# Optimization experiments

Measured on AMD Instinct MI355X. Metric: run time of the kernel, lower is better.

## Reference

```python
import jax, jax.numpy as jnp
import numpy as np

B, T, D, H = 4, 2048, 1024, 16
HD = D // H  # 64
NEG = -np.finfo(np.float32).max


def setup_inputs() -> dict:
    key = jax.random.key(0)
    ks = jax.random.split(key, 9)
    s = 1.0 / np.sqrt(D)
    return {
        "x": jax.random.normal(ks[0], (B, T, D), jnp.float32),
        "wq": jax.random.normal(ks[1], (D, D), jnp.float32) * s,
        "bq": jax.random.normal(ks[2], (D,), jnp.float32) * 0.02,
        "wk": jax.random.normal(ks[3], (D, D), jnp.float32) * s,
        "bk": jax.random.normal(ks[4], (D,), jnp.float32) * 0.02,
        "wv": jax.random.normal(ks[5], (D, D), jnp.float32) * s,
        "bv": jax.random.normal(ks[6], (D,), jnp.float32) * 0.02,
        "wo": jax.random.normal(ks[7], (D, D), jnp.float32) * s,
        "bo": jax.random.normal(ks[8], (D,), jnp.float32) * 0.02,
    }


def reference(x, wq, bq, wk, bk, wv, bv, wo, bo):
    b, t, d = x.shape
    # separate Q, K, V projections, reshape to (B, H, T, HD)
    def proj(w, bias):
        y = x @ w + bias
        return y.reshape(b, t, H, HD).transpose(0, 2, 1, 3)
    q = proj(wq, bq)
    k = proj(wk, bk)
    v = proj(wv, bv)
    scale = 1.0 / np.sqrt(HD).astype(np.float32)
    scores = jnp.einsum("bhqd,bhkd->bhqk", q, k) * scale  # (B,H,T,T)
    # causal mask: -max_float on strictly upper triangle (matches source)
    mask = jnp.triu(jnp.full((t, t), NEG, jnp.float32), k=1)
    attn = jax.nn.softmax(scores + mask, axis=-1)
    out = jnp.einsum("bhqk,bhkd->bhqd", attn, v)
    out = out.transpose(0, 2, 1, 3).reshape(b, t, d)
    return out @ wo + bo
```

## Files before the change

kernel.cpp:

```cpp
#include <hip/hip_runtime.h>

typedef __bf16 bf16x8 __attribute__((ext_vector_type(8)));
typedef float f32x4 __attribute__((ext_vector_type(4)));

#define B_ 4
#define T_ 2048
#define D_ 1024
#define H_ 16
#define HD_ 64
#define M_ 8192
#define QSCALE 0.1803368801111204f

__device__ __forceinline__ ushort f2b(float f) {
  union { float f; unsigned u; } v; v.f = f;
  unsigned u = v.u;
  return (ushort)((u + 0x7FFFu + ((u >> 16) & 1u)) >> 16);
}

__device__ __forceinline__ unsigned pkbf(float a, float b) {
  union { float f; unsigned u; } va, vb; va.f = a; vb.f = b;
  return __builtin_amdgcn_perm(vb.u + 0x8000u, va.u + 0x8000u, 0x07060302u);
}

__device__ __forceinline__ void gll16(const void* g, void* l) {
  __builtin_amdgcn_global_load_lds(
      (const __attribute__((address_space(1))) unsigned*)g,
      (__attribute__((address_space(3))) unsigned*)l, 16, 0, 0);
}

__global__ __launch_bounds__(256) void cast_x_kernel(const float* __restrict__ x,
                                                     ushort* __restrict__ xb) {
  int idx = blockIdx.x * 256 + threadIdx.x;
  float4 v = ((const float4*)x)[idx];
  ushort4 o;
  o.x = f2b(v.x); o.y = f2b(v.y); o.z = f2b(v.z); o.w = f2b(v.w);
  ((ushort4*)xb)[idx] = o;
}

__global__ __launch_bounds__(256) void transpose_w_kernel(
    const float* __restrict__ wq, const float* __restrict__ wk,
    const float* __restrict__ wv, const float* __restrict__ wo,
    ushort* __restrict__ wt_qkv, ushort* __restrict__ wt_o) {
  __shared__ float tile[32][33];
  int z = blockIdx.z;
  const float* src = (z == 0) ? wq : (z == 1) ? wk : (z == 2) ? wv : wo;
  ushort* dst = (z < 3) ? (wt_qkv + (size_t)z * D_ * D_) : wt_o;
  int n0 = blockIdx.x * 32, k0 = blockIdx.y * 32;
  int tx = threadIdx.x & 31, ty = threadIdx.x >> 5;
  for (int i = 0; i < 4; i++) {
    int r = ty + i * 8;
    tile[r][tx] = src[(size_t)(k0 + r) * D_ + n0 + tx];
  }
  __syncthreads();
  for (int i = 0; i < 4; i++) {
    int r = ty + i * 8;
    dst[(size_t)(n0 + r) * D_ + k0 + tx] = f2b(tile[tx][r]);
  }
}

__global__ __launch_bounds__(256) void gemm_kernel(
    const ushort* __restrict__ A, const ushort* __restrict__ Bt, int mode,
    const float* __restrict__ bias_q, const float* __restrict__ bias_k,
    const float* __restrict__ bias_v,
    ushort* __restrict__ qb, ushort* __restrict__ kb, ushort* __restrict__ vtb,
    float* __restrict__ outf) {
  __shared__ ushort As[2][128][64];
  __shared__ ushort Bs[2][128][64];
  int tid = threadIdx.x;
  int wave = tid >> 6, lane = tid & 63, lrow = lane >> 4, lcol = lane & 15;

  int gx = gridDim.x;
  int nwg = gx * gridDim.y;
  int orig = blockIdx.x + gx * blockIdx.y;
  int work = (orig & 7) * (nwg >> 3) + (orig >> 3);
  int m0 = (work / gx) * 128, n0 = (work % gx) * 128;
  int wm = (wave & 1) * 64, wn = (wave >> 1) * 64;

  int rb = tid >> 3;
  int dc = tid & 7;
  int scv = dc ^ (rb & 7);
  const ushort* aBase = A + (size_t)(m0 + rb) * D_ + scv * 8;
  const ushort* bBase = Bt + (size_t)(n0 + rb) * D_ + scv * 8;

  f32x4 zero = {0.f, 0.f, 0.f, 0.f};
  f32x4 acc[4][4];
  for (int i = 0; i < 4; i++)
    for (int j = 0; j < 4; j++) acc[i][j] = zero;

  int swz = lcol & 7;

  auto stage = [&](int buf, int k) {
#pragma unroll
    for (int g = 0; g < 4; g++) {
      gll16(aBase + (size_t)(32 * g) * D_ + k, &As[buf][0][0] + tid * 8 + g * 2048);
      gll16(bBase + (size_t)(32 * g) * D_ + k, &Bs[buf][0][0] + tid * 8 + g * 2048);
    }
  };

  stage(0, 0);

  for (int k0 = 0; k0 < D_; k0 += 64) {
    int cur = (k0 >> 6) & 1, nxt = cur ^ 1;
    __syncthreads();
    if (k0 + 64 < D_) stage(nxt, k0 + 64);

    for (int ks = 0; ks < 2; ks++) {
      bf16x8 af[4], bf[4];
      int ch = ((ks * 4 + lrow) ^ swz) * 8;
      for (int mt = 0; mt < 4; mt++)
        af[mt] = *(const bf16x8*)&As[cur][wm + mt * 16 + lcol][ch];
      for (int nt = 0; nt < 4; nt++)
        bf[nt] = *(const bf16x8*)&Bs[cur][wn + nt * 16 + lcol][ch];
      for (int mt = 0; mt < 4; mt++)
        for (int nt = 0; nt < 4; nt++)
          acc[mt][nt] = __builtin_amdgcn_mfma_f32_16x16x32_bf16(
              af[mt], bf[nt], acc[mt][nt], 0, 0, 0);
    }
  }

  if (mode == 0) {
    int proj = n0 >> 10;
    const float* bias = (proj == 0) ? bias_q : (proj == 1) ? bias_k : bias_v;
    if (proj < 2) {
      ushort* dst = (proj == 0) ? qb : kb;
      bool isq = (proj == 0);
      int c0 = lcol & 1, c1 = lcol & 2;
      for (int mt = 0; mt < 4; mt++) {
        int gm0 = m0 + wm + mt * 16 + lrow * 4;
        int t = gm0 + (lcol & 3);
        int b = t >> 11, tp = t & 2047;
        for (int nt = 0; nt < 4; nt++) {
          int gn = n0 + wn + nt * 16 + lcol;
          int inner = gn & 1023;
          float bv = bias[inner];
          float v0 = acc[mt][nt][0] + bv, v1 = acc[mt][nt][1] + bv;
          float v2 = acc[mt][nt][2] + bv, v3 = acc[mt][nt][3] + bv;
          if (isq) { v0 *= QSCALE; v1 *= QSCALE; v2 *= QSCALE; v3 *= QSCALE; }
          unsigned p0 = ((unsigned)f2b(v1) << 16) | f2b(v0);
          unsigned p1 = ((unsigned)f2b(v3) << 16) | f2b(v2);
          unsigned x0 = __shfl_xor(p0, 1), x1 = __shfl_xor(p1, 1);
          unsigned a0 = c0 ? __builtin_amdgcn_perm(p0, x0, 0x07060302u)
                           : __builtin_amdgcn_perm(x0, p0, 0x05040100u);
          unsigned a1 = c0 ? __builtin_amdgcn_perm(p1, x1, 0x07060302u)
                           : __builtin_amdgcn_perm(x1, p1, 0x05040100u);
          unsigned y0 = __shfl_xor(a0, 2), y1 = __shfl_xor(a1, 2);
          uint2 q2;
          q2.x = c1 ? y1 : a0;
          q2.y = c1 ? a1 : y0;
          int innerb = (n0 + wn + nt * 16 + (lcol & ~3)) & 1023;
          int h = innerb >> 6, hd0 = innerb & 63;
          *(uint2*)&dst[((size_t)(b * H_ + h) * T_ + tp) * HD_ + hd0] = q2;
        }
      }
    } else {
      for (int mt = 0; mt < 4; mt++) {
        int gm0 = m0 + wm + mt * 16 + lrow * 4;
        int b = gm0 >> 11, tp = gm0 & 2047;
        for (int nt = 0; nt < 4; nt++) {
          int gn = n0 + wn + nt * 16 + lcol;
          int inner = gn & 1023;
          int h = inner >> 6, hd = inner & 63;
          float bv = bias[inner];
          ushort4 pk;
          pk.x = f2b(acc[mt][nt][0] + bv);
          pk.y = f2b(acc[mt][nt][1] + bv);
          pk.z = f2b(acc[mt][nt][2] + bv);
          pk.w = f2b(acc[mt][nt][3] + bv);
          *(ushort4*)&vtb[((size_t)(b * H_ + h) * HD_ + hd) * T_ + tp] = pk;
        }
      }
    }
  } else {
    for (int mt = 0; mt < 4; mt++) {
      int gm0 = m0 + wm + mt * 16 + lrow * 4;
      for (int nt = 0; nt < 4; nt++) {
        int gn = n0 + wn + nt * 16 + lcol;
        float bv = bias_q[gn];
        for (int r = 0; r < 4; r++)
          outf[(size_t)(gm0 + r) * D_ + gn] = acc[mt][nt][r] + bv;
      }
    }
  }
}

#define QCOMP(qblk_, q0w_, qfv, accOv, accSv)                                   \
  do {                                                                          \
    f32x4 st[2][4];                                                             \
    for (int qh = 0; qh < 2; qh++)                                              \
      for (int mt = 0; mt < 4; mt++) st[qh][mt] = zero;                         \
    __builtin_amdgcn_s_setprio(1);                                              \
    _Pragma("unroll")                                                           \
    for (int ks = 0; ks < 2; ks++)                                              \
      _Pragma("unroll")                                                         \
      for (int mt = 0; mt < 4; mt++) {                                          \
        bf16x8 kf = *(const bf16x8*)&Ks2[cur][mt * 16 + lcol]                   \
                                        [((ks * 4 + lrow) ^ rsw) * 8];          \
        st[0][mt] = __builtin_amdgcn_mfma_f32_16x16x32_bf16(kf, qfv[0][ks],     \
                                                            st[0][mt], 0, 0, 0);\
        st[1][mt] = __builtin_amdgcn_mfma_f32_16x16x32_bf16(kf, qfv[1][ks],     \
                                                            st[1][mt], 0, 0, 0);\
      }                                                                         \
    __builtin_amdgcn_s_setprio(0);                                              \
    if (j >= 2 * (qblk_)) {                                                     \
      _Pragma("unroll")                                                         \
      for (int qh = 0; qh < 2; qh++) {                                          \
        int q_g = (q0w_) + qh * 16 + lcol;                                      \
        _Pragma("unroll")                                                       \
        for (int mt = 0; mt < 4; mt++)                                          \
          for (int r = 0; r < 4; r++) {                                         \
            int kv_g = j * 64 + mt * 16 + lrow * 4 + r;                         \
            if (kv_g > q_g) st[qh][mt][r] = -1e30f;                             \
          }                                                                     \
      }                                                                         \
    }                                                                           \
    _Pragma("unroll")                                                           \
    for (int qh = 0; qh < 2; qh++)                                              \
      for (int mt = 0; mt < 4; mt++)                                            \
        for (int r = 0; r < 4; r++)                                             \
          st[qh][mt][r] = __builtin_amdgcn_exp2f(st[qh][mt][r]);                \
    _Pragma("unroll")                                                           \
    for (int qh = 0; qh < 2; qh++)                                              \
      for (int mt = 0; mt < 4; mt++) {                                          \
        uint2 pk;                                                               \
        pk.x = pkbf(st[qh][mt][0], st[qh][mt][1]);                              \
        pk.y = pkbf(st[qh][mt][2], st[qh][mt][3]);                              \
        int sl = ((2 * mt + (lrow >> 1)) ^ rsw) * 8 + (lrow & 1) * 4;           \
        *(uint2*)&Ps[wave][qh * 16 + lcol][sl] = pk;                            \
      }                                                                         \
    __builtin_amdgcn_s_setprio(1);                                              \
    _Pragma("unroll")                                                           \
    for (int ks = 0; ks < 2; ks++) {                                            \
      int ch = ((ks * 4 + lrow) ^ rsw) * 8;                                     \
      bf16x8 pf0 = *(const bf16x8*)&Ps[wave][lcol][ch];                         \
      bf16x8 pf1 = *(const bf16x8*)&Ps[wave][16 + lcol][ch];                    \
      accSv[0] = __builtin_amdgcn_mfma_f32_16x16x32_bf16(af1, pf0, accSv[0],    \
                                                         0, 0, 0);              \
      accSv[1] = __builtin_amdgcn_mfma_f32_16x16x32_bf16(af1, pf1, accSv[1],    \
                                                         0, 0, 0);              \
      _Pragma("unroll")                                                         \
      for (int mt = 0; mt < 4; mt++) {                                          \
        bf16x8 vf = *(const bf16x8*)&Vs2[cur][mt * 16 + lcol][ch];              \
        accOv[0][mt] = __builtin_amdgcn_mfma_f32_16x16x32_bf16(vf, pf0,         \
                                                    accOv[0][mt], 0, 0, 0);     \
        accOv[1][mt] = __builtin_amdgcn_mfma_f32_16x16x32_bf16(vf, pf1,         \
                                                    accOv[1][mt], 0, 0, 0);     \
      }                                                                         \
    }                                                                           \
    __builtin_amdgcn_s_setprio(0);                                              \
  } while (0)

__global__ __launch_bounds__(256) void flash_kernel(
    const ushort* __restrict__ qb, const ushort* __restrict__ kb,
    const ushort* __restrict__ vtb, ushort* __restrict__ ob) {
  __shared__ ushort Ks2[2][64][64];
  __shared__ ushort Vs2[2][64][64];
  __shared__ ushort Ps[4][32][64];
  int tid = threadIdx.x;
  int wave = tid >> 6, lane = tid & 63, lrow = lane >> 4, lcol = lane & 15;

  int bid = blockIdx.x + (blockIdx.y << 3);
  int xcd = bid & 7;
  int slot = bid >> 3;
  int phase = slot >> 5;
  int j5 = slot & 31;
  int pm = j5 & 7;
  int bh = xcd * 8 + (j5 >> 3) + phase * 4;
  int p = phase ? 7 - pm : pm;
  int qbA = 15 - p, qbB = p;
  int b = bh >> 4, h = bh & 15;
  const ushort* qp = qb + (size_t)bh * T_ * HD_;
  const ushort* kh = kb + (size_t)bh * T_ * HD_;
  const ushort* vh = vtb + (size_t)bh * HD_ * T_;

  int njA = 2 * qbA + 2, njB = 2 * qbB + 2;

  int r0 = tid >> 3, dc = tid & 7;
  int wsl = (dc ^ (r0 & 7)) * 8;
  int rsw = lcol & 7;

  uint4 kr0, kr1, vr0, vr1;
  auto gload = [&](int jt) {
    kr0 = *(const uint4*)&kh[(size_t)(jt * 64 + r0) * HD_ + dc * 8];
    kr1 = *(const uint4*)&kh[(size_t)(jt * 64 + r0 + 32) * HD_ + dc * 8];
    vr0 = *(const uint4*)&vh[(size_t)r0 * T_ + jt * 64 + dc * 8];
    vr1 = *(const uint4*)&vh[(size_t)(r0 + 32) * T_ + jt * 64 + dc * 8];
  };
  auto swrite = [&](int buf) {
    *(uint4*)&Ks2[buf][r0][wsl] = kr0;
    *(uint4*)&Ks2[buf][r0 + 32][wsl] = kr1;
    *(uint4*)&Vs2[buf][r0][wsl] = vr0;
    *(uint4*)&Vs2[buf][r0 + 32][wsl] = vr1;
  };

  bf16x8 af1;
  {
    __bf16 ov = (__bf16)((lcol == 0) ? 1.0f : 0.0f);
    for (int i2 = 0; i2 < 8; i2++) af1[i2] = ov;
  }

  f32x4 zero = {0.f, 0.f, 0.f, 0.f};

  gload(0);
  swrite(0);
  gload(1);
  __syncthreads();

  int q0wA = qbA * 128 + wave * 32, q0wB = qbB * 128 + wave * 32;
  bf16x8 qfA[2][2], qfB[2][2];
#pragma unroll
  for (int qh = 0; qh < 2; qh++)
#pragma unroll
    for (int ks = 0; ks < 2; ks++) {
      qfA[qh][ks] = *(const bf16x8*)&qp[(size_t)(q0wA + qh * 16 + lcol) * HD_ +
                                        ks * 32 + lrow * 8];
      qfB[qh][ks] = *(const bf16x8*)&qp[(size_t)(q0wB + qh * 16 + lcol) * HD_ +
                                        ks * 32 + lrow * 8];
    }

  f32x4 accOA[2][4], accOB[2][4];
  f32x4 accSA[2], accSB[2];
#pragma unroll
  for (int qh = 0; qh < 2; qh++) {
    accSA[qh] = zero; accSB[qh] = zero;
    for (int mt = 0; mt < 4; mt++) { accOA[qh][mt] = zero; accOB[qh][mt] = zero; }
  }

  for (int j = 0; j < njA; j++) {
    int cur = j & 1;
    if (j * 64 <= q0wA + 31) QCOMP(qbA, q0wA, qfA, accOA, accSA);
    if (j * 64 <= q0wB + 31) QCOMP(qbB, q0wB, qfB, accOB, accSB);
    if (j + 1 < njA) swrite(cur ^ 1);
    if (j + 2 < njA) gload(j + 2);
    __syncthreads();
  }
  (void)njB;

#pragma unroll
  for (int qh = 0; qh < 2; qh++) {
    float lsum = __shfl(accSA[qh][0], lcol);
    float linv = 1.f / lsum;
    int t = q0wA + qh * 16 + lcol;
    size_t base2 = ((size_t)b * T_ + t) * D_ + h * HD_;
#pragma unroll
    for (int mt = 0; mt < 4; mt++) {
      uint2 pk;
      pk.x = pkbf(accOA[qh][mt][0] * linv, accOA[qh][mt][1] * linv);
      pk.y = pkbf(accOA[qh][mt][2] * linv, accOA[qh][mt][3] * linv);
      *(uint2*)&ob[base2 + mt * 16 + lrow * 4] = pk;
    }
  }
#pragma unroll
  for (int qh = 0; qh < 2; qh++) {
    float lsum = __shfl(accSB[qh][0], lcol);
    float linv = 1.f / lsum;
    int t = q0wB + qh * 16 + lcol;
    size_t base2 = ((size_t)b * T_ + t) * D_ + h * HD_;
#pragma unroll
    for (int mt = 0; mt < 4; mt++) {
      uint2 pk;
      pk.x = pkbf(accOB[qh][mt][0] * linv, accOB[qh][mt][1] * linv);
      pk.y = pkbf(accOB[qh][mt][2] * linv, accOB[qh][mt][3] * linv);
      *(uint2*)&ob[base2 + mt * 16 + lrow * 4] = pk;
    }
  }
}

extern "C" void kernel_launch(void* const* d_in, const int* in_sizes, int n_in,
                              void* d_out, int out_size, void* d_ws, size_t ws_size,
                              hipStream_t stream) {
  (void)in_sizes; (void)n_in; (void)out_size; (void)ws_size;
  const float* x  = (const float*)d_in[0];
  const float* wq = (const float*)d_in[1];
  const float* bq = (const float*)d_in[2];
  const float* wk = (const float*)d_in[3];
  const float* bk = (const float*)d_in[4];
  const float* wv = (const float*)d_in[5];
  const float* bv = (const float*)d_in[6];
  const float* wo = (const float*)d_in[7];
  const float* bo = (const float*)d_in[8];
  float* out = (float*)d_out;

  char* ws = (char*)d_ws;
  ushort* xb     = (ushort*)(ws);
  ushort* wt_qkv = (ushort*)(ws + 16777216);
  ushort* wt_o   = (ushort*)(ws + 23068672);
  ushort* qb     = (ushort*)(ws + 25165824);
  ushort* kb     = (ushort*)(ws + 41943040);
  ushort* vtb    = (ushort*)(ws + 58720256);
  ushort* ob     = (ushort*)(ws + 75497472);

  cast_x_kernel<<<8192, 256, 0, stream>>>(x, xb);
  transpose_w_kernel<<<dim3(32, 32, 4), 256, 0, stream>>>(wq, wk, wv, wo, wt_qkv, wt_o);
  gemm_kernel<<<dim3(24, 64), 256, 0, stream>>>(xb, wt_qkv, 0, bq, bk, bv, qb, kb, vtb, nullptr);
  flash_kernel<<<dim3(8, 64), 256, 0, stream>>>(qb, kb, vtb, ob);
  gemm_kernel<<<dim3(8, 64), 256, 0, stream>>>(ob, wt_o, 1, bo, nullptr, nullptr,
                                               nullptr, nullptr, nullptr, out);
}
```

Measured before the change: 246.8 us.

## Restructure GEMM to 256x128 tiles with 8 waves and triple-buffered LDS pipeline

The projection GEMM moves from 128x128 tiles with 4 waves and double buffering to 256x128 tiles with 8 waves, using 144KB of dynamic LDS split into three stages. Global-to-LDS loads are issued two stages ahead and interleaved with the fragment reads, with explicit vmcnt waits, barriers and MFMA priority bumps. This is meant to hide load latency and raise B-tile reuse. The Q/K epilogue drops the shuffle-based packing and uses scalar 2-byte stores instead, which may cost store efficiency, and the large LDS footprint limits occupancy to one block per CU.

```diff
diff --git a/kernel.cpp b/kernel.cpp
--- a/kernel.cpp
+++ b/kernel.cpp
@@ -58,29 +58,42 @@
   }
 }
 
-__global__ __launch_bounds__(256) void gemm_kernel(
+__global__ __launch_bounds__(512) void gemm_kernel(
     const ushort* __restrict__ A, const ushort* __restrict__ Bt, int mode,
     const float* __restrict__ bias_q, const float* __restrict__ bias_k,
     const float* __restrict__ bias_v,
     ushort* __restrict__ qb, ushort* __restrict__ kb, ushort* __restrict__ vtb,
     float* __restrict__ outf) {
-  __shared__ ushort As[2][128][64];
-  __shared__ ushort Bs[2][128][64];
+  extern __shared__ char lds_raw[];
+  ushort (*As)[256][64] = (ushort (*)[256][64])lds_raw;
+  ushort (*Bs)[128][64] = (ushort (*)[128][64])(lds_raw + 98304);
   int tid = threadIdx.x;
   int wave = tid >> 6, lane = tid & 63, lrow = lane >> 4, lcol = lane & 15;
+  int wr = wave >> 1, wc = wave & 1;
 
   int gx = gridDim.x;
   int nwg = gx * gridDim.y;
   int orig = blockIdx.x + gx * blockIdx.y;
   int work = (orig & 7) * (nwg >> 3) + (orig >> 3);
-  int m0 = (work / gx) * 128, n0 = (work % gx) * 128;
-  int wm = (wave & 1) * 64, wn = (wave >> 1) * 64;
-
-  int rb = tid >> 3;
-  int dc = tid & 7;
-  int scv = dc ^ (rb & 7);
-  const ushort* aBase = A + (size_t)(m0 + rb) * D_ + scv * 8;
-  const ushort* bBase = Bt + (size_t)(n0 + rb) * D_ + scv * 8;
+  int m0 = (work / gx) * 256, n0 = (work % gx) * 128;
+
+  int r_s = tid >> 3, c_s = tid & 7;
+  int scv = c_s ^ (r_s & 7);
+  const ushort* aB = A + (size_t)(m0 + r_s) * D_ + scv * 8;
+  const ushort* bB = Bt + (size_t)(n0 + r_s) * D_ + scv * 8;
+
+  auto stageA = [&](int buf, int t, int u) {
+    const ushort* s = aB + (size_t)u * 128 * D_ + t * 64;
+    char* d = (char*)&As[buf][0][0] + u * 16384 + tid * 16;
+    gll16(s, d);
+    gll16(s + (size_t)64 * D_, d + 8192);
+  };
+  auto stageB = [&](int buf, int t) {
+    const ushort* s = bB + t * 64;
+    char* d = (char*)&Bs[buf][0][0] + tid * 16;
+    gll16(s, d);
+    gll16(s + (size_t)64 * D_, d + 8192);
+  };
 
   f32x4 zero = {0.f, 0.f, 0.f, 0.f};
   f32x4 acc[4][4];
@@ -89,78 +102,73 @@
 
   int swz = lcol & 7;
 
-  auto stage = [&](int buf, int k) {
-#pragma unroll
-    for (int g = 0; g < 4; g++) {
-      gll16(aBase + (size_t)(32 * g) * D_ + k, &As[buf][0][0] + tid * 8 + g * 2048);
-      gll16(bBase + (size_t)(32 * g) * D_ + k, &Bs[buf][0][0] + tid * 8 + g * 2048);
-    }
-  };
-
-  stage(0, 0);
-
-  for (int k0 = 0; k0 < D_; k0 += 64) {
-    int cur = (k0 >> 6) & 1, nxt = cur ^ 1;
-    __syncthreads();
-    if (k0 + 64 < D_) stage(nxt, k0 + 64);
-
-    for (int ks = 0; ks < 2; ks++) {
+  stageA(0, 0, 0); stageA(0, 0, 1); stageB(0, 0);
+  stageA(1, 1, 0); stageA(1, 1, 1); stageB(1, 1);
+  asm volatile("s_waitcnt vmcnt(6)" ::: "memory");
+  __builtin_amdgcn_sched_barrier(0);
+  __builtin_amdgcn_s_barrier();
+
+#pragma unroll
+  for (int t = 0; t < 16; ++t) {
+    int buf = t % 3;
+    int nb = (t + 2) % 3;
+#pragma unroll
+    for (int ks = 0; ks < 2; ++ks) {
       bf16x8 af[4], bf[4];
       int ch = ((ks * 4 + lrow) ^ swz) * 8;
+#pragma unroll
       for (int mt = 0; mt < 4; mt++)
-        af[mt] = *(const bf16x8*)&As[cur][wm + mt * 16 + lcol][ch];
+        af[mt] = *(const bf16x8*)&As[buf][wr * 64 + mt * 16 + lcol][ch];
+#pragma unroll
       for (int nt = 0; nt < 4; nt++)
-        bf[nt] = *(const bf16x8*)&Bs[cur][wn + nt * 16 + lcol][ch];
+        bf[nt] = *(const bf16x8*)&Bs[buf][wc * 64 + nt * 16 + lcol][ch];
+      if (t + 2 < 16) {
+        if (ks == 0) { stageA(nb, t + 2, 0); stageA(nb, t + 2, 1); }
+        else         { stageB(nb, t + 2); }
+      }
+      __builtin_amdgcn_sched_barrier(0);
+      __builtin_amdgcn_s_barrier();
+      __builtin_amdgcn_sched_barrier(0);
+      __builtin_amdgcn_s_setprio(1);
+#pragma unroll
       for (int mt = 0; mt < 4; mt++)
+#pragma unroll
         for (int nt = 0; nt < 4; nt++)
           acc[mt][nt] = __builtin_amdgcn_mfma_f32_16x16x32_bf16(
               af[mt], bf[nt], acc[mt][nt], 0, 0, 0);
+      __builtin_amdgcn_s_setprio(0);
+      if (ks == 1) {
+        if (t <= 13) {
+          asm volatile("s_waitcnt vmcnt(6)" ::: "memory");
+        } else if (t == 14) {
+          asm volatile("s_waitcnt vmcnt(0)" ::: "memory");
+        }
+      }
+      __builtin_amdgcn_sched_barrier(0);
+      __builtin_amdgcn_s_barrier();
     }
   }
 
   if (mode == 0) {
     int proj = n0 >> 10;
     const float* bias = (proj == 0) ? bias_q : (proj == 1) ? bias_k : bias_v;
-    if (proj < 2) {
-      ushort* dst = (proj == 0) ? qb : kb;
-      bool isq = (proj == 0);
-      int c0 = lcol & 1, c1 = lcol & 2;
-      for (int mt = 0; mt < 4; mt++) {
-        int gm0 = m0 + wm + mt * 16 + lrow * 4;
-        int t = gm0 + (lcol & 3);
-        int b = t >> 11, tp = t & 2047;
-        for (int nt = 0; nt < 4; nt++) {
-          int gn = n0 + wn + nt * 16 + lcol;
-          int inner = gn & 1023;
-          float bv = bias[inner];
-          float v0 = acc[mt][nt][0] + bv, v1 = acc[mt][nt][1] + bv;
-          float v2 = acc[mt][nt][2] + bv, v3 = acc[mt][nt][3] + bv;
-          if (isq) { v0 *= QSCALE; v1 *= QSCALE; v2 *= QSCALE; v3 *= QSCALE; }
-          unsigned p0 = ((unsigned)f2b(v1) << 16) | f2b(v0);
-          unsigned p1 = ((unsigned)f2b(v3) << 16) | f2b(v2);
-          unsigned x0 = __shfl_xor(p0, 1), x1 = __shfl_xor(p1, 1);
-          unsigned a0 = c0 ? __builtin_amdgcn_perm(p0, x0, 0x07060302u)
-                           : __builtin_amdgcn_perm(x0, p0, 0x05040100u);
-          unsigned a1 = c0 ? __builtin_amdgcn_perm(p1, x1, 0x07060302u)
-                           : __builtin_amdgcn_perm(x1, p1, 0x05040100u);
-          unsigned y0 = __shfl_xor(a0, 2), y1 = __shfl_xor(a1, 2);
-          uint2 q2;
-          q2.x = c1 ? y1 : a0;
-          q2.y = c1 ? a1 : y0;
-          int innerb = (n0 + wn + nt * 16 + (lcol & ~3)) & 1023;
-          int h = innerb >> 6, hd0 = innerb & 63;
-          *(uint2*)&dst[((size_t)(b * H_ + h) * T_ + tp) * HD_ + hd0] = q2;
-        }
-      }
-    } else {
-      for (int mt = 0; mt < 4; mt++) {
-        int gm0 = m0 + wm + mt * 16 + lrow * 4;
-        int b = gm0 >> 11, tp = gm0 & 2047;
-        for (int nt = 0; nt < 4; nt++) {
-          int gn = n0 + wn + nt * 16 + lcol;
-          int inner = gn & 1023;
-          int h = inner >> 6, hd = inner & 63;
-          float bv = bias[inner];
+    for (int mt = 0; mt < 4; mt++) {
+      int gm0 = m0 + wr * 64 + mt * 16 + lrow * 4;
+      int b = gm0 >> 11, tp = gm0 & 2047;
+      for (int nt = 0; nt < 4; nt++) {
+        int gn = n0 + wc * 64 + nt * 16 + lcol;
+        int inner = gn & 1023;
+        int h = inner >> 6, hd = inner & 63;
+        float bv = bias[inner];
+        if (proj == 0) {
+          size_t base = ((size_t)(b * H_ + h) * T_ + tp) * HD_ + hd;
+          for (int r = 0; r < 4; r++)
+            qb[base + (size_t)r * HD_] = f2b((acc[mt][nt][r] + bv) * QSCALE);
+        } else if (proj == 1) {
+          size_t base = ((size_t)(b * H_ + h) * T_ + tp) * HD_ + hd;
+          for (int r = 0; r < 4; r++)
+            kb[base + (size_t)r * HD_] = f2b(acc[mt][nt][r] + bv);
+        } else {
           ushort4 pk;
           pk.x = f2b(acc[mt][nt][0] + bv);
           pk.y = f2b(acc[mt][nt][1] + bv);
@@ -172,9 +180,9 @@
     }
   } else {
     for (int mt = 0; mt < 4; mt++) {
-      int gm0 = m0 + wm + mt * 16 + lrow * 4;
+      int gm0 = m0 + wr * 64 + mt * 16 + lrow * 4;
       for (int nt = 0; nt < 4; nt++) {
-        int gn = n0 + wn + nt * 16 + lcol;
+        int gn = n0 + wc * 64 + nt * 16 + lcol;
         float bv = bias_q[gn];
         for (int r = 0; r < 4; r++)
           outf[(size_t)(gm0 + r) * D_ + gn] = acc[mt][nt][r] + bv;
@@ -389,10 +397,13 @@
   ushort* vtb    = (ushort*)(ws + 58720256);
   ushort* ob     = (ushort*)(ws + 75497472);
 
+  hipFuncSetAttribute((const void*)gemm_kernel,
+                      hipFuncAttributeMaxDynamicSharedMemorySize, 147456);
+
   cast_x_kernel<<<8192, 256, 0, stream>>>(x, xb);
   transpose_w_kernel<<<dim3(32, 32, 4), 256, 0, stream>>>(wq, wk, wv, wo, wt_qkv, wt_o);
-  gemm_kernel<<<dim3(24, 64), 256, 0, stream>>>(xb, wt_qkv, 0, bq, bk, bv, qb, kb, vtb, nullptr);
+  gemm_kernel<<<dim3(24, 32), 512, 147456, stream>>>(xb, wt_qkv, 0, bq, bk, bv, qb, kb, vtb, nullptr);
   flash_kernel<<<dim3(8, 64), 256, 0, stream>>>(qb, kb, vtb, ob);
-  gemm_kernel<<<dim3(8, 64), 256, 0, stream>>>(ob, wt_o, 1, bo, nullptr, nullptr,
-                                               nullptr, nullptr, nullptr, out);
-}
+  gemm_kernel<<<dim3(8, 32), 512, 147456, stream>>>(ob, wt_o, 1, bo, nullptr, nullptr,
+                                                    nullptr, nullptr, nullptr, out);
+}
```

Measured after the change: 256.8 us. +4.0%, slower.
